# Kernel optimization log

Measured on AMD Instinct MI355X. Metric: run time of the kernel, lower is better.

## Reference

```python
import jax, jax.numpy as jnp
import numpy as np

N_NODES = 40000
N_EDGES = 320000
IN_DIM = 256
HID = 128
HEADS = 4
N_GAT = 3  # num_layers - 1
EPS = 1e-5
NEG_SLOPE = 0.2  # PyG GATConv default


def setup_inputs() -> dict:
    key = jax.random.key(0)
    ks = jax.random.split(key, 16)
    s = 0.05
    return {
        "x": jax.random.normal(ks[0], (N_NODES, IN_DIM), jnp.float32),
        "edge_index": jax.random.randint(ks[1], (2, N_EDGES), 0, N_NODES, jnp.int64),
        "proj_W": jax.random.normal(ks[2], (IN_DIM, HID), jnp.float32) * s,
        "proj_b": jnp.zeros((HID,), jnp.float32),
        "gat_W": jax.random.normal(ks[3], (N_GAT, HID, HEADS * HID), jnp.float32) * s,
        "gat_att_src": jax.random.normal(ks[4], (N_GAT, HEADS, HID), jnp.float32) * s,
        "gat_att_dst": jax.random.normal(ks[5], (N_GAT, HEADS, HID), jnp.float32) * s,
        "gat_bias": jnp.zeros((N_GAT, HID), jnp.float32),
        "ln_gamma": jnp.ones((N_GAT, HID), jnp.float32),
        "ln_beta": jnp.zeros((N_GAT, HID), jnp.float32),
        "gcn_W": jax.random.normal(ks[6], (HID, 1), jnp.float32) * s,
        "gcn_b": jnp.zeros((1,), jnp.float32),
    }


def reference(x, edge_index, proj_W, proj_b, gat_W, gat_att_src, gat_att_dst,
              gat_bias, ln_gamma, ln_beta, gcn_W, gcn_b):
    N = x.shape[0]
    loops = jnp.arange(N)
    src = jnp.concatenate([edge_index[0], loops])  # add_self_loops=True
    dst = jnp.concatenate([edge_index[1], loops])

    h = x @ proj_W + proj_b  # [N, HID]

    for i in range(N_GAT):
        identity = h
        xh = (h @ gat_W[i]).reshape(N, HEADS, HID)      # [N, H, C]
        a_s = jnp.einsum("nhc,hc->nh", xh, gat_att_src[i])  # [N, H]
        a_d = jnp.einsum("nhc,hc->nh", xh, gat_att_dst[i])
        e = jax.nn.leaky_relu(a_s[src] + a_d[dst], NEG_SLOPE)  # [E, H]
        # segment softmax over incoming edges per dst node
        m = jax.ops.segment_max(e, dst, num_segments=N)
        ex = jnp.exp(e - m[dst])
        denom = jax.ops.segment_sum(ex, dst, num_segments=N)
        alpha = ex / denom[dst]                         # [E, H]
        agg = jax.ops.segment_sum(xh[src] * alpha[:, :, None], dst, num_segments=N)
        h = agg.mean(axis=1) + gat_bias[i]              # concat=False -> head mean
        # LayerNorm (biased variance, eps=1e-5)
        mu = h.mean(-1, keepdims=True)
        var = ((h - mu) ** 2).mean(-1, keepdims=True)
        h = (h - mu) * jax.lax.rsqrt(var + EPS) * ln_gamma[i] + ln_beta[i]
        h = jax.nn.relu(h)
        # dropout: inference mode -> identity
        h = h + identity

    # GCNConv(hidden, 1) with symmetric normalization and self loops
    deg = jax.ops.segment_sum(jnp.ones_like(dst, dtype=h.dtype), dst, num_segments=N)
    dinv = jax.lax.rsqrt(deg)  # deg >= 1 due to self loops
    norm = dinv[src] * dinv[dst]                        # [E]
    xw = h @ gcn_W                                      # [N, 1]
    out = jax.ops.segment_sum(xw[src] * norm[:, None], dst, num_segments=N) + gcn_b
    return jax.nn.sigmoid(out).reshape(-1)
```

## Files before the change

### kernel.cpp

```cpp
#include <hip/hip_runtime.h>
#include <math.h>

#define INDIM 256
#define HID 128
#define HEADS 4
#define NGAT 3
#define LN_EPS 1e-5f
#define SLOPE 0.2f
#define MPAD 40064
#define LOG2E 1.4426950408889634f

typedef __attribute__((ext_vector_type(8))) short short8;
typedef __attribute__((ext_vector_type(4))) float f32x4;

__device__ inline float wsum(float v) {
#pragma unroll
  for (int m = 1; m < 64; m <<= 1) v += __shfl_xor(v, m, 64);
  return v;
}
__device__ inline float wmax(float v) {
#pragma unroll
  for (int m = 1; m < 64; m <<= 1) v = fmaxf(v, __shfl_xor(v, m, 64));
  return v;
}
__device__ inline float lk2(float v) { return fmaxf(v, SLOPE * v) * LOG2E; }
__device__ inline float sel4(float a0, float a1, float a2, float a3, int i) {
  float lo = (i & 1) ? a1 : a0;
  float hi = (i & 1) ? a3 : a2;
  return (i & 2) ? hi : lo;
}

__device__ inline unsigned short f2b(float f) {
  unsigned u = __float_as_uint(f);
  unsigned r = (u + 0x7FFFu + ((u >> 16) & 1u)) >> 16;
  return (unsigned short)r;
}
__device__ inline float b2f(unsigned short b) {
  return __uint_as_float(((unsigned)b) << 16);
}
__device__ inline void unp8(const uint4 v, float f[8]) {
  f[0] = __uint_as_float(v.x << 16);
  f[1] = __uint_as_float(v.x & 0xFFFF0000u);
  f[2] = __uint_as_float(v.y << 16);
  f[3] = __uint_as_float(v.y & 0xFFFF0000u);
  f[4] = __uint_as_float(v.z << 16);
  f[5] = __uint_as_float(v.z & 0xFFFF0000u);
  f[6] = __uint_as_float(v.w << 16);
  f[7] = __uint_as_float(v.w & 0xFFFF0000u);
}

__device__ __host__ inline size_t fidx(int row, int k, int K) {
  return ((size_t)(row >> 4) * (K >> 5) + (k >> 5)) * 512 +
         ((((k >> 3) & 3) * 16 + (row & 15)) << 3) + (k & 7);
}

__global__ void k_deg(const int* __restrict__ ei, int E, int N, int* __restrict__ deg) {
  int e = blockIdx.x * blockDim.x + threadIdx.x;
  if (e >= E + N) return;
  int dst = (e < E) ? ei[E + e] : (e - E);
  atomicAdd(&deg[dst], 1);
}

__global__ void k_scan1(const int* __restrict__ deg, int N, int* __restrict__ bsums) {
  __shared__ int s[256];
  int gid = blockIdx.x * 256 + threadIdx.x;
  s[threadIdx.x] = (gid < N) ? deg[gid] : 0;
  __syncthreads();
  for (int off = 128; off > 0; off >>= 1) {
    if (threadIdx.x < off) s[threadIdx.x] += s[threadIdx.x + off];
    __syncthreads();
  }
  if (threadIdx.x == 0) bsums[blockIdx.x] = s[0];
}

__global__ void k_scan2(int* __restrict__ bsums, int nblk, int* __restrict__ rowptr, int N) {
  __shared__ int s[256];
  int t = threadIdx.x;
  int v = (t < nblk) ? bsums[t] : 0;
  s[t] = v;
  __syncthreads();
  for (int off = 1; off < 256; off <<= 1) {
    int u = (t >= off) ? s[t - off] : 0;
    __syncthreads();
    s[t] += u;
    __syncthreads();
  }
  if (t < nblk) bsums[t] = s[t] - v;
  if (t == nblk - 1) rowptr[N] = s[t];
}

__global__ void k_scan3(const int* __restrict__ deg, int N, const int* __restrict__ bsums,
                        int* __restrict__ rowptr, int* __restrict__ cursor,
                        float* __restrict__ dinv) {
  __shared__ int s[256];
  int gid = blockIdx.x * 256 + threadIdx.x;
  int v = (gid < N) ? deg[gid] : 0;
  s[threadIdx.x] = v;
  __syncthreads();
  for (int off = 1; off < 256; off <<= 1) {
    int t = (threadIdx.x >= off) ? s[threadIdx.x - off] : 0;
    __syncthreads();
    s[threadIdx.x] += t;
    __syncthreads();
  }
  if (gid < N) {
    int ex = bsums[blockIdx.x] + s[threadIdx.x] - v;
    rowptr[gid] = ex;
    cursor[gid] = ex;
    dinv[gid] = rsqrtf((float)v);
  }
}

__global__ void k_fill(const int* __restrict__ ei, int E, int N,
                       int* __restrict__ cursor, int* __restrict__ csr) {
  int e = blockIdx.x * blockDim.x + threadIdx.x;
  if (e >= E + N) return;
  int src, dst;
  if (e < E) { src = ei[e]; dst = ei[E + e]; } else { src = dst = e - E; }
  int pos = atomicAdd(&cursor[dst], 1);
  csr[pos] = src;
}

__global__ void k_wprep(const float* __restrict__ Wp, const float* __restrict__ Wg,
                        unsigned short* __restrict__ WtPF,
                        unsigned short* __restrict__ Wt2F) {
  int idx = blockIdx.x * 256 + threadIdx.x;
  if (idx < INDIM * HID) {
    int k = idx >> 7, c = idx & 127;
    WtPF[fidx(c, k, INDIM)] = f2b(Wp[idx]);
    return;
  }
  idx -= INDIM * HID;
  if (idx >= NGAT * HID * HEADS * HID) return;
  int l = idx / (HID * HEADS * HID);
  int rem = idx - l * HID * HEADS * HID;
  int k = rem >> 9;
  int cc = rem & 511;
  int hh = cc >> 7, c = cc & 127;
  Wt2F[(size_t)l * (HID * HEADS * HID) + fidx(c, hh * HID + k, HEADS * HID)] =
      f2b(Wg[idx] * 0.25f);
}

__global__ void k_wvec(const float* __restrict__ W, const float* __restrict__ atts,
                       const float* __restrict__ attd, float* __restrict__ w_s,
                       float* __restrict__ w_d) {
  int lane = threadIdx.x & 63;
  int idx = blockIdx.x * 4 + (threadIdx.x >> 6);
  if (idx >= NGAT * HEADS * HID) return;
  int l = idx / (HEADS * HID);
  int rem = idx - l * (HEADS * HID);
  int hh = rem >> 7, k = rem & 127;
  const float2 w2 = *(const float2*)(W + ((size_t)(l * HID + k)) * (HEADS * HID) +
                                     hh * HID + lane * 2);
  const float2 s2 = *(const float2*)(atts + (size_t)(l * HEADS + hh) * HID + lane * 2);
  const float2 d2 = *(const float2*)(attd + (size_t)(l * HEADS + hh) * HID + lane * 2);
  float ps = w2.x * s2.x + w2.y * s2.y;
  float pd = w2.x * d2.x + w2.y * d2.y;
  ps = wsum(ps);
  pd = wsum(pd);
  if (lane == 0) { w_s[idx] = ps; w_d[idx] = pd; }
}

__global__ __launch_bounds__(256) void k_mm(
    const float* __restrict__ x, const unsigned short* __restrict__ WtPF,
    const float* __restrict__ bias, const float* __restrict__ ws0,
    const float* __restrict__ wd0, unsigned short* __restrict__ hb,
    float* __restrict__ a_s, float* __restrict__ a_d, int Mreal) {
  __shared__ unsigned short As[64 * INDIM];
  const int wid = threadIdx.x >> 6;
  const int lane = threadIdx.x & 63;
  const int l15 = lane & 15;
  const int g = lane >> 4;
  const int row0 = blockIdx.x * 64 + wid * 16;
#pragma unroll
  for (int i = 0; i < 8; ++i) {
    int p = threadIdx.x + 256 * i;
    int nl = p >> 5, kc = p & 31;
    int grow = blockIdx.x * 64 + nl;
    uint4 pk = make_uint4(0, 0, 0, 0);
    if (grow < Mreal) {
      const float* ap = x + (size_t)grow * INDIM + kc * 8;
      float4 u = *(const float4*)ap;
      float4 v = *(const float4*)(ap + 4);
      pk.x = (unsigned)f2b(u.x) | ((unsigned)f2b(u.y) << 16);
      pk.y = (unsigned)f2b(u.z) | ((unsigned)f2b(u.w) << 16);
      pk.z = (unsigned)f2b(v.x) | ((unsigned)f2b(v.y) << 16);
      pk.w = (unsigned)f2b(v.z) | ((unsigned)f2b(v.w) << 16);
    }
    *(uint4*)&As[((nl >> 4) * 8 + (kc >> 2)) * 512 + (((kc & 3) * 16 + (nl & 15)) << 3)] = pk;
  }
  __syncthreads();
  f32x4 acc[8] = {};
  const unsigned short* Bp = WtPF + lane * 8;
  for (int kb = 0; kb < 8; ++kb) {
    short8 af = *(const short8*)&As[(wid * 8 + kb) * 512 + lane * 8];
    short8 bfr[8];
#pragma unroll
    for (int ni = 0; ni < 8; ++ni)
      bfr[ni] = *(const short8*)(Bp + (size_t)(ni * 8 + kb) * 512);
#pragma unroll
    for (int ni = 0; ni < 8; ++ni)
      acc[ni] = __builtin_amdgcn_mfma_f32_16x16x32_bf16(af, bfr[ni], acc[ni], 0, 0, 0);
  }
#pragma unroll
  for (int r = 0; r < 4; ++r) {
    const int row = row0 + g * 4 + r;
    unsigned short* hbr = hb + (size_t)row * HID;
    float yv[8];
#pragma unroll
    for (int ni = 0; ni < 8; ++ni) {
      const int c = ni * 16 + l15;
      yv[ni] = acc[ni][r] + bias[c];
      hbr[c] = f2b(yv[ni]);
    }
    float ps[4], pd[4];
#pragma unroll
    for (int h4 = 0; h4 < 4; ++h4) {
      float pv = 0.f, qv = 0.f;
#pragma unroll
      for (int ni = 0; ni < 8; ++ni) {
        const int c = h4 * HID + ni * 16 + l15;
        pv = fmaf(yv[ni], ws0[c], pv);
        qv = fmaf(yv[ni], wd0[c], qv);
      }
#pragma unroll
      for (int m = 1; m < 16; m <<= 1) {
        pv += __shfl_xor(pv, m, 64);
        qv += __shfl_xor(qv, m, 64);
      }
      ps[h4] = pv;
      pd[h4] = qv;
    }
    if (l15 == 0) {
      *(float4*)(a_s + (size_t)row * 4) = make_float4(ps[0], ps[1], ps[2], ps[3]);
      *(float4*)(a_d + (size_t)row * 4) = make_float4(pd[0], pd[1], pd[2], pd[3]);
    }
  }
}

__global__ __launch_bounds__(256) void k_agg2(
    const int* __restrict__ rowptr, const int* __restrict__ csr,
    const unsigned short* __restrict__ hb, const float* __restrict__ a_s,
    const float* __restrict__ a_d, unsigned short* __restrict__ aggF, int N) {
  __shared__ int s_lds[4][64];
  __shared__ float al_lds[4][4][68];
  int lane = threadIdx.x & 63;
  int wid = threadIdx.x >> 6;
  int n = blockIdx.x * 4 + wid;
  if (n >= MPAD) return;
  const int g = lane >> 4;
  const int l15 = lane & 15;
  size_t oaddr = ((size_t)(n >> 4) * 16 + (g * 4 + (l15 >> 2))) * 512 +
                 (((l15 & 3) * 16 + (n & 15)) << 3);
  if (n >= N) {
    *(uint4*)(aggF + oaddr) = make_uint4(0, 0, 0, 0);
    return;
  }
  int beg = rowptr[n], end = rowptr[n + 1];
  int deg = end - beg;
  const unsigned short* hbase = hb + l15 * 8;
  float acc[8] = {};
  float f[8];
  if (deg <= 64) {
    const float ad = a_d[n * 4 + g];
    int sj[4];
    float ex[4];
    float mymax = -3e38f;
#pragma unroll
    for (int j = 0; j < 4; ++j) {
      int e = beg + l15 + 16 * j;
      bool v = e < end;
      int s = v ? csr[e] : 0;
      sj[j] = s;
      float Lv = v ? lk2(a_s[s * 4 + g] + ad) : -3e38f;
      ex[j] = Lv;
      mymax = fmaxf(mymax, Lv);
    }
#pragma unroll
    for (int m = 1; m < 16; m <<= 1) mymax = fmaxf(mymax, __shfl_xor(mymax, m, 64));
    float mysum = 0.f;
#pragma unroll
    for (int j = 0; j < 4; ++j) {
      ex[j] = exp2f(ex[j] - mymax);
      mysum += ex[j];
    }
#pragma unroll
    for (int m = 1; m < 16; m <<= 1) mysum += __shfl_xor(mysum, m, 64);
    float r = 1.f / mysum;
#pragma unroll
    for (int j = 0; j < 4; ++j) {
      int i = l15 + 16 * j;
      al_lds[wid][g][i] = ex[j] * r;
      if (g == 0) s_lds[wid][i] = sj[j];
    }
    asm volatile("s_waitcnt lgkmcnt(0)" ::: "memory");
    const int* sw = s_lds[wid];
    const float* aw = al_lds[wid][g];
    int nIter = (deg + 3) >> 2;
    for (int it = 0; it < nIter; ++it) {
      int4 s4 = *(const int4*)(sw + it * 4);
      float4 a4 = *(const float4*)(aw + it * 4);
      uint4 r0 = *(const uint4*)(hbase + (size_t)s4.x * HID);
      uint4 r1 = *(const uint4*)(hbase + (size_t)s4.y * HID);
      uint4 r2 = *(const uint4*)(hbase + (size_t)s4.z * HID);
      uint4 r3 = *(const uint4*)(hbase + (size_t)s4.w * HID);
      unp8(r0, f);
#pragma unroll
      for (int j = 0; j < 8; ++j) acc[j] = fmaf(a4.x, f[j], acc[j]);
      unp8(r1, f);
#pragma unroll
      for (int j = 0; j < 8; ++j) acc[j] = fmaf(a4.y, f[j], acc[j]);
      unp8(r2, f);
#pragma unroll
      for (int j = 0; j < 8; ++j) acc[j] = fmaf(a4.z, f[j], acc[j]);
      unp8(r3, f);
#pragma unroll
      for (int j = 0; j < 8; ++j) acc[j] = fmaf(a4.w, f[j], acc[j]);
    }
  } else {
    const float4 adv = *(const float4*)(a_d + (size_t)n * 4);
    float m0 = -3e38f, m1 = -3e38f, m2 = -3e38f, m3 = -3e38f;
    for (int e = beg + lane; e < end; e += 64) {
      int s = csr[e];
      const float4 asv = *(const float4*)(a_s + (size_t)s * 4);
      m0 = fmaxf(m0, lk2(asv.x + adv.x));
      m1 = fmaxf(m1, lk2(asv.y + adv.y));
      m2 = fmaxf(m2, lk2(asv.z + adv.z));
      m3 = fmaxf(m3, lk2(asv.w + adv.w));
    }
    m0 = wmax(m0); m1 = wmax(m1); m2 = wmax(m2); m3 = wmax(m3);
    float d0 = 0.f, d1 = 0.f, d2 = 0.f, d3 = 0.f;
    for (int e = beg + lane; e < end; e += 64) {
      int s = csr[e];
      const float4 asv = *(const float4*)(a_s + (size_t)s * 4);
      d0 += exp2f(lk2(asv.x + adv.x) - m0);
      d1 += exp2f(lk2(asv.y + adv.y) - m1);
      d2 += exp2f(lk2(asv.z + adv.z) - m2);
      d3 += exp2f(lk2(asv.w + adv.w) - m3);
    }
    float r0 = 1.f / wsum(d0);
    float r1 = 1.f / wsum(d1);
    float r2 = 1.f / wsum(d2);
    float r3 = 1.f / wsum(d3);
    for (int sb = beg; sb < end; sb += 64) {
      int e = sb + lane;
      bool val = e < end;
      int s = csr[val ? e : end - 1];
      const float4 asv = *(const float4*)(a_s + (size_t)s * 4);
      float q0 = val ? exp2f(lk2(asv.x + adv.x) - m0) * r0 : 0.f;
      float q1 = val ? exp2f(lk2(asv.y + adv.y) - m1) * r1 : 0.f;
      float q2 = val ? exp2f(lk2(asv.z + adv.z) - m2) * r2 : 0.f;
      float q3 = val ? exp2f(lk2(asv.w + adv.w) - m3) * r3 : 0.f;
      int cnt = min(64, end - sb);
      for (int i = 0; i < cnt; ++i) {
        int si = __shfl(s, i, 64);
        float c0 = __shfl(q0, i, 64), c1 = __shfl(q1, i, 64);
        float c2 = __shfl(q2, i, 64), c3 = __shfl(q3, i, 64);
        uint4 hv = *(const uint4*)(hbase + (size_t)si * HID);
        float bi = sel4(c0, c1, c2, c3, g);
        unp8(hv, f);
#pragma unroll
        for (int j = 0; j < 8; ++j) acc[j] = fmaf(bi, f[j], acc[j]);
      }
    }
  }
  uint4 pk;
  pk.x = (unsigned)f2b(acc[0]) | ((unsigned)f2b(acc[1]) << 16);
  pk.y = (unsigned)f2b(acc[2]) | ((unsigned)f2b(acc[3]) << 16);
  pk.z = (unsigned)f2b(acc[4]) | ((unsigned)f2b(acc[5]) << 16);
  pk.w = (unsigned)f2b(acc[6]) | ((unsigned)f2b(acc[7]) << 16);
  *(uint4*)(aggF + oaddr) = pk;
}

template <int ATT>
__global__ __launch_bounds__(256) void k_mm2(
    const unsigned short* __restrict__ aggF, const unsigned short* __restrict__ Bt,
    const float* __restrict__ bias, const float* __restrict__ gamma,
    const float* __restrict__ beta, const float* __restrict__ wsn,
    const float* __restrict__ wdn, unsigned short* __restrict__ hb,
    float* __restrict__ a_s, float* __restrict__ a_d,
    const float* __restrict__ dinvp, float* __restrict__ xwd) {
  __shared__ float red[4][16][132];
  const int wid = threadIdx.x >> 6;
  const int lane = threadIdx.x & 63;
  const int l15 = lane & 15;
  const int g = lane >> 4;
  const int row0 = blockIdx.x * 16;
  f32x4 acc[8] = {};
  const unsigned short* Ap = aggF + (size_t)blockIdx.x * 16 * 512 + lane * 8;
  const unsigned short* Bp = Bt + lane * 8;
#pragma unroll
  for (int kq = 0; kq < 4; ++kq) {
    const int kb = wid * 4 + kq;
    short8 a0 = *(const short8*)(Ap + (size_t)kb * 512);
    short8 bfr[8];
#pragma unroll
    for (int ni = 0; ni < 8; ++ni)
      bfr[ni] = *(const short8*)(Bp + (size_t)(ni * 16 + kb) * 512);
#pragma unroll
    for (int ni = 0; ni < 8; ++ni)
      acc[ni] = __builtin_amdgcn_mfma_f32_16x16x32_bf16(a0, bfr[ni], acc[ni], 0, 0, 0);
  }
#pragma unroll
  for (int ni = 0; ni < 8; ++ni)
#pragma unroll
    for (int r = 0; r < 4; ++r)
      red[wid][g * 4 + r][ni * 16 + l15] = acc[ni][r];
  __syncthreads();
  const int row_l = threadIdx.x >> 4;
  const int cg = threadIdx.x & 15;
  const int c0 = cg * 8;
  const int row = row0 + row_l;
  float y[8];
#pragma unroll
  for (int j = 0; j < 8; ++j)
    y[j] = ((red[0][row_l][c0 + j] + red[1][row_l][c0 + j]) +
            (red[2][row_l][c0 + j] + red[3][row_l][c0 + j])) + bias[c0 + j];
  float s = 0.f;
#pragma unroll
  for (int j = 0; j < 8; ++j) s += y[j];
#pragma unroll
  for (int m = 1; m < 16; m <<= 1) s += __shfl_xor(s, m, 64);
  float mu = s * (1.f / 128.f);
  float q = 0.f;
#pragma unroll
  for (int j = 0; j < 8; ++j) {
    float dd = y[j] - mu;
    q += dd * dd;
  }
#pragma unroll
  for (int m = 1; m < 16; m <<= 1) q += __shfl_xor(q, m, 64);
  float rstd = rsqrtf(q * (1.f / 128.f) + LN_EPS);
  unsigned short* hbr = hb + (size_t)row * HID;
  uint4 hv = *(const uint4*)(hbr + c0);
  float res[8];
  unp8(hv, res);
  float yv[8];
#pragma unroll
  for (int j = 0; j < 8; ++j) {
    float t = (y[j] - mu) * rstd * gamma[c0 + j] + beta[c0 + j];
    yv[j] = fmaxf(t, 0.f) + res[j];
  }
  uint4 pk;
  pk.x = (unsigned)f2b(yv[0]) | ((unsigned)f2b(yv[1]) << 16);
  pk.y = (unsigned)f2b(yv[2]) | ((unsigned)f2b(yv[3]) << 16);
  pk.z = (unsigned)f2b(yv[4]) | ((unsigned)f2b(yv[5]) << 16);
  pk.w = (unsigned)f2b(yv[6]) | ((unsigned)f2b(yv[7]) << 16);
  *(uint4*)(hbr + c0) = pk;
  if (ATT == 1) {
    float ps[4], pd[4];
#pragma unroll
    for (int h4 = 0; h4 < 4; ++h4) {
      float pv = 0.f, qv = 0.f;
#pragma unroll
      for (int j = 0; j < 8; ++j) {
        const int c = h4 * HID + c0 + j;
        pv = fmaf(yv[j], wsn[c], pv);
        qv = fmaf(yv[j], wdn[c], qv);
      }
#pragma unroll
      for (int m = 1; m < 16; m <<= 1) {
        pv += __shfl_xor(pv, m, 64);
        qv += __shfl_xor(qv, m, 64);
      }
      ps[h4] = pv;
      pd[h4] = qv;
    }
    if (cg == 0) {
      *(float4*)(a_s + (size_t)row * 4) = make_float4(ps[0], ps[1], ps[2], ps[3]);
      *(float4*)(a_d + (size_t)row * 4) = make_float4(pd[0], pd[1], pd[2], pd[3]);
    }
  } else {
    float pv = 0.f;
#pragma unroll
    for (int j = 0; j < 8; ++j) pv = fmaf(yv[j], wsn[c0 + j], pv);
#pragma unroll
    for (int m = 1; m < 16; m <<= 1) pv += __shfl_xor(pv, m, 64);
    if (cg == 0) xwd[row] = pv * dinvp[row];
  }
}

__global__ __launch_bounds__(256) void k_gcn(const int* __restrict__ rowptr,
                                             const int* __restrict__ csr,
                                             const float* __restrict__ xwd,
                                             const float* __restrict__ dinv,
                                             const float* __restrict__ gcn_b,
                                             float* __restrict__ out, int N) {
  int n = blockIdx.x * blockDim.x + threadIdx.x;
  if (n >= N) return;
  float acc = 0.f;
  int beg = rowptr[n], end = rowptr[n + 1];
  int e = beg;
  for (; e + 4 <= end; e += 4) {
    int s0 = csr[e], s1 = csr[e + 1], s2 = csr[e + 2], s3 = csr[e + 3];
    float v0 = xwd[s0], v1 = xwd[s1], v2 = xwd[s2], v3 = xwd[s3];
    acc += (v0 + v1) + (v2 + v3);
  }
  for (; e < end; ++e) acc += xwd[csr[e]];
  float z = acc * dinv[n] + gcn_b[0];
  out[n] = 1.f / (1.f + expf(-z));
}

extern "C" void kernel_launch(void* const* d_in, const int* in_sizes, int n_in,
                              void* d_out, int out_size, void* d_ws, size_t ws_size,
                              hipStream_t stream) {
  const float* x = (const float*)d_in[0];
  const int* ei = (const int*)d_in[1];
  const float* proj_W = (const float*)d_in[2];
  const float* proj_b = (const float*)d_in[3];
  const float* gat_W = (const float*)d_in[4];
  const float* gat_as = (const float*)d_in[5];
  const float* gat_ad = (const float*)d_in[6];
  const float* gat_bias = (const float*)d_in[7];
  const float* ln_g = (const float*)d_in[8];
  const float* ln_b = (const float*)d_in[9];
  const float* gcn_W = (const float*)d_in[10];
  const float* gcn_b = (const float*)d_in[11];
  float* out = (float*)d_out;

  const int N = in_sizes[0] / INDIM;
  const int E = in_sizes[1] / 2;
  const int TOT = E + N;

  size_t off = 0;
  auto alloc = [&](size_t bytes) {
    void* p = (char*)d_ws + off;
    off += (bytes + 255) & ~(size_t)255;
    return p;
  };
  unsigned short* hb = (unsigned short*)alloc((size_t)MPAD * HID * 2);
  unsigned short* aggF = (unsigned short*)alloc((size_t)MPAD * HEADS * HID * 2);
  unsigned short* WtPF = (unsigned short*)alloc((size_t)HID * INDIM * 2);
  unsigned short* Wt2F = (unsigned short*)alloc((size_t)NGAT * HID * HEADS * HID * 2);
  float* w_s = (float*)alloc((size_t)NGAT * HEADS * HID * 4);
  float* w_d = (float*)alloc((size_t)NGAT * HEADS * HID * 4);
  float* a_s = (float*)alloc((size_t)MPAD * HEADS * 4);
  float* a_d = (float*)alloc((size_t)MPAD * HEADS * 4);
  int* deg = (int*)alloc((size_t)N * 4);
  int* rowptr = (int*)alloc((size_t)(N + 1) * 4);
  int* cursor = (int*)alloc((size_t)N * 4);
  int* csr = (int*)alloc((size_t)TOT * 4);
  int* bsums = (int*)alloc(1024);
  float* dinv = (float*)alloc((size_t)MPAD * 4);
  float* xwd = (float*)alloc((size_t)MPAD * 4);
  (void)ws_size;

  const int NBLK = (N + 255) / 256;
  const int EBLK = (TOT + 255) / 256;

  hipMemsetAsync(deg, 0, (size_t)N * 4, stream);
  k_deg<<<EBLK, 256, 0, stream>>>(ei, E, N, deg);
  k_scan1<<<NBLK, 256, 0, stream>>>(deg, N, bsums);
  k_scan2<<<1, 256, 0, stream>>>(bsums, NBLK, rowptr, N);
  k_scan3<<<NBLK, 256, 0, stream>>>(deg, N, bsums, rowptr, cursor, dinv);
  k_fill<<<EBLK, 256, 0, stream>>>(ei, E, N, cursor, csr);

  const int WPN = INDIM * HID + NGAT * HID * HEADS * HID;
  k_wprep<<<(WPN + 255) / 256, 256, 0, stream>>>(proj_W, gat_W, WtPF, Wt2F);
  k_wvec<<<(NGAT * HEADS * HID + 3) / 4, 256, 0, stream>>>(gat_W, gat_as, gat_ad, w_s, w_d);

  k_mm<<<MPAD / 64, 256, 0, stream>>>(x, WtPF, proj_b, w_s, w_d, hb, a_s, a_d, N);

  for (int i = 0; i < NGAT; ++i) {
    k_agg2<<<MPAD / 4, 256, 0, stream>>>(rowptr, csr, hb, a_s, a_d, aggF, N);
    if (i < NGAT - 1) {
      k_mm2<1><<<MPAD / 16, 256, 0, stream>>>(
          aggF, Wt2F + (size_t)i * HID * HEADS * HID, gat_bias + (size_t)i * HID,
          ln_g + (size_t)i * HID, ln_b + (size_t)i * HID,
          w_s + (size_t)(i + 1) * HEADS * HID, w_d + (size_t)(i + 1) * HEADS * HID,
          hb, a_s, a_d, nullptr, nullptr);
    } else {
      k_mm2<2><<<MPAD / 16, 256, 0, stream>>>(
          aggF, Wt2F + (size_t)i * HID * HEADS * HID, gat_bias + (size_t)i * HID,
          ln_g + (size_t)i * HID, ln_b + (size_t)i * HID, gcn_W, nullptr,
          hb, nullptr, nullptr, dinv, xwd);
    }
  }

  k_gcn<<<NBLK, 256, 0, stream>>>(rowptr, csr, xwd, dinv, gcn_b, out, N);
}
```

Baseline: 247.5 us.

## Split each node's aggregation across two waves with LDS reduction

The GAT aggregation kernel now assigns two wavefronts per destination node. Each handles half of the up-to-64 neighbor edges, and the partial sums are combined through shared memory before the bf16 write. The aim is more parallelism and shorter per-wave gather chains. In exchange it doubles the launched blocks, computes the softmax redundantly in both waves, and adds a block barrier. For typical low degrees the second wave does no gather work at all.

```diff
diff --git a/kernel.cpp b/kernel.cpp
--- a/kernel.cpp
+++ b/kernel.cpp
@@ -242,26 +242,26 @@
     const int* __restrict__ rowptr, const int* __restrict__ csr,
     const unsigned short* __restrict__ hb, const float* __restrict__ a_s,
     const float* __restrict__ a_d, unsigned short* __restrict__ aggF, int N) {
-  __shared__ int s_lds[4][64];
-  __shared__ float al_lds[4][4][68];
+  __shared__ int s_lds[4][32];
+  __shared__ float al_lds[4][4][36];
+  __shared__ float red[2][64][8];
   int lane = threadIdx.x & 63;
   int wid = threadIdx.x >> 6;
-  int n = blockIdx.x * 4 + wid;
-  if (n >= MPAD) return;
+  int n = blockIdx.x * 2 + (wid >> 1);
+  const int half = wid & 1;
   const int g = lane >> 4;
   const int l15 = lane & 15;
-  size_t oaddr = ((size_t)(n >> 4) * 16 + (g * 4 + (l15 >> 2))) * 512 +
-                 (((l15 & 3) * 16 + (n & 15)) << 3);
-  if (n >= N) {
-    *(uint4*)(aggF + oaddr) = make_uint4(0, 0, 0, 0);
-    return;
-  }
-  int beg = rowptr[n], end = rowptr[n + 1];
-  int deg = end - beg;
+  const bool valid = n < N;
+  int beg = 0, end = 0, deg = 0;
+  if (valid) {
+    beg = rowptr[n];
+    end = rowptr[n + 1];
+    deg = end - beg;
+  }
   const unsigned short* hbase = hb + l15 * 8;
   float acc[8] = {};
   float f[8];
-  if (deg <= 64) {
+  if (valid && deg <= 64) {
     const float ad = a_d[n * 4 + g];
     int sj[4];
     float ex[4];
@@ -288,15 +288,18 @@
     for (int m = 1; m < 16; m <<= 1) mysum += __shfl_xor(mysum, m, 64);
     float r = 1.f / mysum;
 #pragma unroll
-    for (int j = 0; j < 4; ++j) {
-      int i = l15 + 16 * j;
+    for (int jj = 0; jj < 2; ++jj) {
+      int j = half * 2 + jj;
+      int i = l15 + 16 * jj;
       al_lds[wid][g][i] = ex[j] * r;
       if (g == 0) s_lds[wid][i] = sj[j];
     }
     asm volatile("s_waitcnt lgkmcnt(0)" ::: "memory");
     const int* sw = s_lds[wid];
     const float* aw = al_lds[wid][g];
-    int nIter = (deg + 3) >> 2;
+    int myc = deg - half * 32;
+    myc = myc < 0 ? 0 : (myc > 32 ? 32 : myc);
+    int nIter = (myc + 3) >> 2;
     for (int it = 0; it < nIter; ++it) {
       int4 s4 = *(const int4*)(sw + it * 4);
       float4 a4 = *(const float4*)(aw + it * 4);
@@ -317,7 +320,7 @@
 #pragma unroll
       for (int j = 0; j < 8; ++j) acc[j] = fmaf(a4.w, f[j], acc[j]);
     }
-  } else {
+  } else if (valid && half == 0) {
     const float4 adv = *(const float4*)(a_d + (size_t)n * 4);
     float m0 = -3e38f, m1 = -3e38f, m2 = -3e38f, m3 = -3e38f;
     for (int e = beg + lane; e < end; e += 64) {
@@ -364,12 +367,24 @@
       }
     }
   }
-  uint4 pk;
-  pk.x = (unsigned)f2b(acc[0]) | ((unsigned)f2b(acc[1]) << 16);
-  pk.y = (unsigned)f2b(acc[2]) | ((unsigned)f2b(acc[3]) << 16);
-  pk.z = (unsigned)f2b(acc[4]) | ((unsigned)f2b(acc[5]) << 16);
-  pk.w = (unsigned)f2b(acc[6]) | ((unsigned)f2b(acc[7]) << 16);
-  *(uint4*)(aggF + oaddr) = pk;
+  const int pair = wid >> 1;
+  if (half == 1) {
+#pragma unroll
+    for (int j = 0; j < 8; ++j) red[pair][lane][j] = acc[j];
+  }
+  __syncthreads();
+  if (half == 0) {
+#pragma unroll
+    for (int j = 0; j < 8; ++j) acc[j] += red[pair][lane][j];
+    uint4 pk;
+    pk.x = (unsigned)f2b(acc[0]) | ((unsigned)f2b(acc[1]) << 16);
+    pk.y = (unsigned)f2b(acc[2]) | ((unsigned)f2b(acc[3]) << 16);
+    pk.z = (unsigned)f2b(acc[4]) | ((unsigned)f2b(acc[5]) << 16);
+    pk.w = (unsigned)f2b(acc[6]) | ((unsigned)f2b(acc[7]) << 16);
+    size_t oaddr = ((size_t)(n >> 4) * 16 + (g * 4 + (l15 >> 2))) * 512 +
+                   (((l15 & 3) * 16 + (n & 15)) << 3);
+    *(uint4*)(aggF + oaddr) = pk;
+  }
 }
 
 template <int ATT>
@@ -562,7 +577,7 @@
   k_mm<<<MPAD / 64, 256, 0, stream>>>(x, WtPF, proj_b, w_s, w_d, hb, a_s, a_d, N);
 
   for (int i = 0; i < NGAT; ++i) {
-    k_agg2<<<MPAD / 4, 256, 0, stream>>>(rowptr, csr, hb, a_s, a_d, aggF, N);
+    k_agg2<<<MPAD / 2, 256, 0, stream>>>(rowptr, csr, hb, a_s, a_d, aggF, N);
     if (i < NGAT - 1) {
       k_mm2<1><<<MPAD / 16, 256, 0, stream>>>(
           aggF, Wt2F + (size_t)i * HID * HEADS * HID, gat_bias + (size_t)i * HID,
```

New measurement: 295.0 us. 1.19x slower.
